# Kernel optimization log

Hardware: AMD Instinct MI355X
Metric: run time of the kernel (lower is better)

Reference implementation:

```python
import jax, jax.numpy as jnp
import numpy as np


def setup_inputs() -> dict:
    key = jax.random.key(0)
    k1, k2, k3, k4 = jax.random.split(key, 4)
    B1, N1, B2, N2, D = 64, 128, 64, 128, 128
    v1 = jax.random.normal(k1, (B1, N1, D), dtype=jnp.float32)
    v2 = jax.random.normal(k2, (B2, N2, D), dtype=jnp.float32)
    sz1 = jax.random.randint(k3, (B1,), 0, 128, dtype=jnp.int64)
    sz2 = jax.random.randint(k4, (B2,), 0, 128, dtype=jnp.int64)
    return {"v1": v1, "sz1": sz1, "v2": v2, "sz2": sz2}


def reference(v1, sz1, v2, sz2):
    # v1: (B1, N1, D) padded node features; v2: (B2, N2, D)
    # Pairwise Euclidean distances dist[b1,b2,i,j] = ||v1[b1,i] - v2[b2,j]||
    # via the gemm identity instead of the original's 5D broadcast.
    x2 = jnp.sum(v1 * v1, axis=-1)                     # (B1, N1)
    y2 = jnp.sum(v2 * v2, axis=-1)                     # (B2, N2)
    xy = jnp.einsum('aid,bjd->abij', v1, v2)           # (B1, B2, N1, N2)
    sq = x2[:, None, :, None] + y2[None, :, None, :] - 2.0 * xy
    dist = jnp.sqrt(jnp.maximum(sq, 0.0))              # (B1, B2, N1, N2)

    N1, N2 = v1.shape[1], v2.shape[1]
    mask1 = jnp.arange(N1)[None, :] >= sz1[:, None]    # (B1, N1) padded v1 nodes
    mask2 = jnp.arange(N2)[None, :] >= sz2[:, None]    # (B2, N2) padded v2 nodes
    mask = mask1[:, None, :, None] | mask2[None, :, None, :]  # (B1, B2, N1, N2)

    # Original fills masked entries with the global max of the (unmasked) distances.
    maximum = dist.max()
    dm = jnp.where(mask, maximum, dist)

    bm1 = dm.min(axis=2)                               # min over v1 nodes -> (B1, B2, N2)
    bm2 = dm.min(axis=3)                               # min over v2 nodes -> (B1, B2, N1)
    bm1 = jnp.where(jnp.all(mask, axis=2), 0.0, bm1)   # zero fully-masked columns
    bm2 = jnp.where(jnp.all(mask, axis=3), 0.0, bm2)   # zero fully-masked rows

    return bm1.sum(axis=2) + bm2.sum(axis=2)           # (B1, B2)
```

## Files before the change

### kernel.cpp

```cpp
#include <hip/hip_runtime.h>
#include <math.h>


typedef __attribute__((ext_vector_type(8))) short short8;
typedef __attribute__((ext_vector_type(4))) float f32x4;
typedef unsigned int u32;
typedef unsigned short ushort_t;

static __device__ __forceinline__ ushort_t f32_to_bf16_rne(float f) {
    u32 b = __float_as_uint(f);
    b += 0x7FFFu + ((b >> 16) & 1u);
    return (ushort_t)(b >> 16);
}

__global__ __launch_bounds__(256) void softhd_pre(
    const float* __restrict__ v1, const float* __restrict__ v2,
    ushort_t* __restrict__ v1b, ushort_t* __restrict__ v2b,
    float* __restrict__ x2g, float* __restrict__ y2g)
{
    int flat = blockIdx.x * 256 + threadIdx.x;
    int c = flat & 15;
    int r = (flat >> 4) & 127;
    int b = (flat >> 11) & 63;
    int t = flat >> 17;

    const float* src = (t ? v2 : v1) + ((size_t)((b << 7) + r) << 7) + c * 8;
    ushort_t* dst = (t ? v2b : v1b) + ((size_t)((b << 7) + r) << 7);

    float4 q0 = *(const float4*)(src);
    float4 q1 = *(const float4*)(src + 4);

    ushort_t h[8];
    h[0] = f32_to_bf16_rne(q0.x); h[1] = f32_to_bf16_rne(q0.y);
    h[2] = f32_to_bf16_rne(q0.z); h[3] = f32_to_bf16_rne(q0.w);
    h[4] = f32_to_bf16_rne(q1.x); h[5] = f32_to_bf16_rne(q1.y);
    h[6] = f32_to_bf16_rne(q1.z); h[7] = f32_to_bf16_rne(q1.w);

    float p = 0.f;
#pragma unroll
    for (int k = 0; k < 8; ++k) {
        float fv = __uint_as_float((u32)h[k] << 16);
        p += fv * fv;
    }

    uint4 w;
    w.x = (u32)h[0] | ((u32)h[1] << 16);
    w.y = (u32)h[2] | ((u32)h[3] << 16);
    w.z = (u32)h[4] | ((u32)h[5] << 16);
    w.w = (u32)h[6] | ((u32)h[7] << 16);
    *(uint4*)(dst + ((c ^ (r & 7)) << 3)) = w;

    p += __shfl_xor(p, 1);
    p += __shfl_xor(p, 2);
    p += __shfl_xor(p, 4);
    p += __shfl_xor(p, 8);
    if (c == 0) (t ? y2g : x2g)[(b << 7) + r] = p;
}

static __device__ __forceinline__ void stage_half(
    const char* g1, const char* g2, ushort_t* s1, ushort_t* s2,
    int tid, int srcoff)
{
#pragma unroll
    for (int it = 0; it < 4; ++it) {
        int m = it * 256 + tid;
        int so = ((m >> 3) << 8) + srcoff + ((m & 7) << 4);
        int dof = m << 4;
        __builtin_amdgcn_global_load_lds(
            (const __attribute__((address_space(1))) u32*)(g1 + so),
            (__attribute__((address_space(3))) u32*)((char*)s1 + dof),
            16, 0, 0);
        __builtin_amdgcn_global_load_lds(
            (const __attribute__((address_space(1))) u32*)(g2 + so),
            (__attribute__((address_space(3))) u32*)((char*)s2 + dof),
            16, 0, 0);
    }
}

__global__ __launch_bounds__(256, 3) void softhd_mfma(
    const ushort_t* __restrict__ v1b, const ushort_t* __restrict__ v2b,
    const float* __restrict__ x2g, const float* __restrict__ y2g,
    const int* __restrict__ sz1, const int* __restrict__ sz2,
    float* __restrict__ out)
{
    __shared__ __align__(16) ushort_t s1[128 * 64];
    __shared__ __align__(16) ushort_t s2[128 * 64];
    __shared__ float sx2[128], sy2[128];
    __shared__ u32 sbm1[128], sbm2[128];
    __shared__ float swsum[4];

    const int tid = threadIdx.x;
    const int lane = tid & 63;
    const int wid = tid >> 6;
    const int bid = ((blockIdx.x & 7) << 9) | (blockIdx.x >> 3);
    const int b1 = bid >> 6, b2 = bid & 63;

    const char* g1 = (const char*)(v1b + ((size_t)b1 << 14));
    const char* g2 = (const char*)(v2b + ((size_t)b2 << 14));

    stage_half(g1, g2, s1, s2, tid, 0);

    if (tid < 128) {
        sx2[tid] = x2g[(b1 << 7) + tid];
        sbm1[tid] = 0x7F800000u;
    } else {
        sy2[tid - 128] = y2g[(b2 << 7) + (tid - 128)];
        sbm2[tid - 128] = 0x7F800000u;
    }
    __syncthreads();

    const int qr = wid >> 1, qc = wid & 1;
    const int ibase = qr << 6, jbase = qc << 6;
    const int rf = lane & 15, kg = lane >> 4;
    const int h = rf & 7;

    const ushort_t* a_base = s1 + ((ibase + rf) << 6);
    const ushort_t* b_base = s2 + ((jbase + rf) << 6);

    f32x4 acc[4][4];
#pragma unroll
    for (int fi = 0; fi < 4; ++fi)
#pragma unroll
        for (int fj = 0; fj < 4; ++fj)
            acc[fi][fj] = (f32x4){0.f, 0.f, 0.f, 0.f};

#pragma unroll
    for (int half = 0; half < 2; ++half) {
        if (half == 1) {
            __syncthreads();
            stage_half(g1, g2, s1, s2, tid, 128);
            __syncthreads();
        }
#pragma unroll
        for (int s = 0; s < 2; ++s) {
            const int p8 = (((s << 2) + kg) ^ h) << 3;
            short8 a[4], b[4];
#pragma unroll
            for (int f = 0; f < 4; ++f) {
                a[f] = *(const short8*)(a_base + (f << 10) + p8);
                b[f] = *(const short8*)(b_base + (f << 10) + p8);
            }
#pragma unroll
            for (int fi = 0; fi < 4; ++fi)
#pragma unroll
                for (int fj = 0; fj < 4; ++fj)
                    acc[fi][fj] = __builtin_amdgcn_mfma_f32_16x16x32_bf16(
                        a[fi], b[fj], acc[fi][fj], 0, 0, 0);
        }
    }

    const int n1 = min(max(sz1[b1], 0), 128);
    const int n2 = min(max(sz2[b2], 0), 128);
    const float INF = __builtin_inff();

    float xie[16], yje[4];
#pragma unroll
    for (int t = 0; t < 16; ++t) {
        int i = ibase + ((t >> 2) << 4) + (kg << 2) + (t & 3);
        xie[t] = (i < n1) ? sx2[i] : INF;
    }
#pragma unroll
    for (int fj = 0; fj < 4; ++fj) {
        int j = jbase + (fj << 4) + rf;
        yje[fj] = (j < n2) ? sy2[j] : INF;
    }

    float minj[4], mini[16];
#pragma unroll
    for (int fj = 0; fj < 4; ++fj) minj[fj] = INF;
#pragma unroll
    for (int t = 0; t < 16; ++t) mini[t] = INF;

#pragma unroll
    for (int fi = 0; fi < 4; ++fi) {
        float u[4][4];
#pragma unroll
        for (int fj = 0; fj < 4; ++fj)
#pragma unroll
            for (int q = 0; q < 4; ++q)
                u[fj][q] = fmaf(acc[fi][fj][q], -2.f, xie[fi * 4 + q] + yje[fj]);
#pragma unroll
        for (int fj = 0; fj < 4; ++fj) {
            minj[fj] = fminf(fminf(minj[fj], u[fj][0]), u[fj][1]);
            minj[fj] = fminf(fminf(minj[fj], u[fj][2]), u[fj][3]);
        }
#pragma unroll
        for (int q = 0; q < 4; ++q) {
            float mt = mini[fi * 4 + q];
            mt = fminf(fminf(mt, u[0][q]), u[1][q]);
            mt = fminf(fminf(mt, u[2][q]), u[3][q]);
            mini[fi * 4 + q] = mt;
        }
    }

#pragma unroll
    for (int k = 0; k < 4; ++k) {
        const int d = 1 << k;
        const bool hi = (lane >> k) & 1;
#pragma unroll
        for (int base = 0; base < 16; base += 2 * (1 << k)) {
            float pa = fminf(mini[base], __shfl_xor(mini[base], d));
            float pb = fminf(mini[base + d], __shfl_xor(mini[base + d], d));
            mini[base] = hi ? pb : pa;
        }
    }
    {
        float dmin = __builtin_amdgcn_sqrtf(fmaxf(mini[0], 0.f));
        int i = ibase + ((rf >> 2) << 4) + (kg << 2) + (rf & 3);
        atomicMin(&sbm2[i], __float_as_uint(dmin));
    }

#pragma unroll
    for (int k = 0; k < 2; ++k) {
        const int d = 16 << k;
        const bool hi = (lane >> (4 + k)) & 1;
#pragma unroll
        for (int base = 0; base < 4; base += 2 * (1 << k)) {
            float pa = fminf(minj[base], __shfl_xor(minj[base], d));
            float pb = fminf(minj[base + (1 << k)],
                             __shfl_xor(minj[base + (1 << k)], d));
            minj[base] = hi ? pb : pa;
        }
    }
    {
        float dmin = __builtin_amdgcn_sqrtf(fmaxf(minj[0], 0.f));
        atomicMin(&sbm1[jbase + lane], __float_as_uint(dmin));
    }
    __syncthreads();

    float v = 0.f;
    if (tid < 128) {
        if (n1 > 0 && tid < n2) v += __uint_as_float(sbm1[tid]);
        if (n2 > 0 && tid < n1) v += __uint_as_float(sbm2[tid]);
    }
#pragma unroll
    for (int off = 32; off >= 1; off >>= 1) v += __shfl_down(v, off);
    if (lane == 0) swsum[wid] = v;
    __syncthreads();
    if (tid == 0) out[bid] = swsum[0] + swsum[1] + swsum[2] + swsum[3];
}

extern "C" void kernel_launch(void* const* d_in, const int* in_sizes, int n_in,
                              void* d_out, int out_size, void* d_ws, size_t ws_size,
                              hipStream_t stream) {
    const float* v1  = (const float*)d_in[0];
    const int*   sz1 = (const int*)d_in[1];
    const float* v2  = (const float*)d_in[2];
    const int*   sz2 = (const int*)d_in[3];
    float* out = (float*)d_out;
    (void)in_sizes; (void)n_in; (void)out_size; (void)ws_size;

    char* ws = (char*)d_ws;
    ushort_t* v1b = (ushort_t*)ws;
    ushort_t* v2b = (ushort_t*)(ws + (2u << 20));
    float*    x2g = (float*)(ws + (4u << 20));
    float*    y2g = x2g + 64 * 128;

    softhd_pre<<<dim3(1024), dim3(256), 0, stream>>>(v1, v2, v1b, v2b, x2g, y2g);
    softhd_mfma<<<dim3(4096), dim3(256), 0, stream>>>(v1b, v2b, x2g, y2g,
                                                      sz1, sz2, out);
}
```

Baseline: 36.55 us.

## Double-buffer K-quarter staging with chunk-major bf16 layout for overlapped LDS loads

The preprocessing kernel now writes bf16 features in a chunk-major layout, so each 32-wide K quarter of a 128-row tile is one contiguous 8KB block. The MFMA kernel splits K into four quarters held in a double-buffered LDS array. It issues the async global-to-LDS load for the next quarter before computing on the current one, which replaces the previous two-half, load-then-sync scheme. The occupancy hint is raised from 3 to 4 blocks, and the size loads are hoisted earlier. This trades more barriers per block for overlap of loads with MFMA work.

```diff
diff --git a/kernel.cpp b/kernel.cpp
--- a/kernel.cpp
+++ b/kernel.cpp
@@ -25,7 +25,7 @@
     int t = flat >> 17;
 
     const float* src = (t ? v2 : v1) + ((size_t)((b << 7) + r) << 7) + c * 8;
-    ushort_t* dst = (t ? v2b : v1b) + ((size_t)((b << 7) + r) << 7);
+    char* dstp = (char*)((t ? v2b : v1b) + ((size_t)b << 14));
 
     float4 q0 = *(const float4*)(src);
     float4 q1 = *(const float4*)(src + 4);
@@ -48,7 +48,9 @@
     w.y = (u32)h[2] | ((u32)h[3] << 16);
     w.z = (u32)h[4] | ((u32)h[5] << 16);
     w.w = (u32)h[6] | ((u32)h[7] << 16);
-    *(uint4*)(dst + ((c ^ (r & 7)) << 3)) = w;
+
+    int off = ((c >> 2) << 13) + ((r >> 3) << 9) + ((c & 3) << 7) + ((r & 7) << 4);
+    *(uint4*)(dstp + off) = w;
 
     p += __shfl_xor(p, 1);
     p += __shfl_xor(p, 2);
@@ -57,34 +59,13 @@
     if (c == 0) (t ? y2g : x2g)[(b << 7) + r] = p;
 }
 
-static __device__ __forceinline__ void stage_half(
-    const char* g1, const char* g2, ushort_t* s1, ushort_t* s2,
-    int tid, int srcoff)
-{
-#pragma unroll
-    for (int it = 0; it < 4; ++it) {
-        int m = it * 256 + tid;
-        int so = ((m >> 3) << 8) + srcoff + ((m & 7) << 4);
-        int dof = m << 4;
-        __builtin_amdgcn_global_load_lds(
-            (const __attribute__((address_space(1))) u32*)(g1 + so),
-            (__attribute__((address_space(3))) u32*)((char*)s1 + dof),
-            16, 0, 0);
-        __builtin_amdgcn_global_load_lds(
-            (const __attribute__((address_space(1))) u32*)(g2 + so),
-            (__attribute__((address_space(3))) u32*)((char*)s2 + dof),
-            16, 0, 0);
-    }
-}
-
-__global__ __launch_bounds__(256, 3) void softhd_mfma(
+__global__ __launch_bounds__(256, 4) void softhd_mfma(
     const ushort_t* __restrict__ v1b, const ushort_t* __restrict__ v2b,
     const float* __restrict__ x2g, const float* __restrict__ y2g,
     const int* __restrict__ sz1, const int* __restrict__ sz2,
     float* __restrict__ out)
 {
-    __shared__ __align__(16) ushort_t s1[128 * 64];
-    __shared__ __align__(16) ushort_t s2[128 * 64];
+    __shared__ __align__(16) ushort_t sb[2][2][4096];
     __shared__ float sx2[128], sy2[128];
     __shared__ u32 sbm1[128], sbm2[128];
     __shared__ float swsum[4];
@@ -95,10 +76,29 @@
     const int bid = ((blockIdx.x & 7) << 9) | (blockIdx.x >> 3);
     const int b1 = bid >> 6, b2 = bid & 63;
 
-    const char* g1 = (const char*)(v1b + ((size_t)b1 << 14));
-    const char* g2 = (const char*)(v2b + ((size_t)b2 << 14));
-
-    stage_half(g1, g2, s1, s2, tid, 0);
+    const char* gp0 = (const char*)(v1b + ((size_t)b1 << 14));
+    const char* gp1 = (const char*)(v2b + ((size_t)b2 << 14));
+
+#define STAGE(d, q)                                                          \
+    {                                                                        \
+        _Pragma("unroll")                                                    \
+        for (int e = 0; e < 2; ++e) {                                        \
+            int m16 = ((e << 8) + tid) << 4;                                 \
+            __builtin_amdgcn_global_load_lds(                                \
+                (const __attribute__((address_space(1))) u32*)(gp0 + ((q) << 13) + m16), \
+                (__attribute__((address_space(3))) u32*)((char*)&sb[d][0][0] + m16),     \
+                16, 0, 0);                                                   \
+            __builtin_amdgcn_global_load_lds(                                \
+                (const __attribute__((address_space(1))) u32*)(gp1 + ((q) << 13) + m16), \
+                (__attribute__((address_space(3))) u32*)((char*)&sb[d][1][0] + m16),     \
+                16, 0, 0);                                                   \
+        }                                                                    \
+    }
+
+    STAGE(0, 0);
+
+    const int n1 = min(max(sz1[b1], 0), 128);
+    const int n2 = min(max(sz2[b2], 0), 128);
 
     if (tid < 128) {
         sx2[tid] = x2g[(b1 << 7) + tid];
@@ -112,10 +112,15 @@
     const int qr = wid >> 1, qc = wid & 1;
     const int ibase = qr << 6, jbase = qc << 6;
     const int rf = lane & 15, kg = lane >> 4;
-    const int h = rf & 7;
-
-    const ushort_t* a_base = s1 + ((ibase + rf) << 6);
-    const ushort_t* b_base = s2 + ((jbase + rf) << 6);
+
+    int aoff[4], boff[4];
+#pragma unroll
+    for (int f = 0; f < 4; ++f) {
+        int ra = ibase + (f << 4) + rf;
+        int rb = jbase + (f << 4) + rf;
+        aoff[f] = ((ra >> 3) << 8) + (kg << 6) + ((ra & 7) << 3);
+        boff[f] = ((rb >> 3) << 8) + (kg << 6) + ((rb & 7) << 3);
+    }
 
     f32x4 acc[4][4];
 #pragma unroll
@@ -125,32 +130,25 @@
             acc[fi][fj] = (f32x4){0.f, 0.f, 0.f, 0.f};
 
 #pragma unroll
-    for (int half = 0; half < 2; ++half) {
-        if (half == 1) {
-            __syncthreads();
-            stage_half(g1, g2, s1, s2, tid, 128);
-            __syncthreads();
-        }
-#pragma unroll
-        for (int s = 0; s < 2; ++s) {
-            const int p8 = (((s << 2) + kg) ^ h) << 3;
-            short8 a[4], b[4];
-#pragma unroll
-            for (int f = 0; f < 4; ++f) {
-                a[f] = *(const short8*)(a_base + (f << 10) + p8);
-                b[f] = *(const short8*)(b_base + (f << 10) + p8);
-            }
-#pragma unroll
-            for (int fi = 0; fi < 4; ++fi)
-#pragma unroll
-                for (int fj = 0; fj < 4; ++fj)
-                    acc[fi][fj] = __builtin_amdgcn_mfma_f32_16x16x32_bf16(
-                        a[fi], b[fj], acc[fi][fj], 0, 0, 0);
-        }
-    }
-
-    const int n1 = min(max(sz1[b1], 0), 128);
-    const int n2 = min(max(sz2[b2], 0), 128);
+    for (int q = 0; q < 4; ++q) {
+        const int d = q & 1;
+        if (q < 3) STAGE(d ^ 1, q + 1);
+        short8 a[4], b[4];
+#pragma unroll
+        for (int f = 0; f < 4; ++f) {
+            a[f] = *(const short8*)(&sb[d][0][0] + aoff[f]);
+            b[f] = *(const short8*)(&sb[d][1][0] + boff[f]);
+        }
+#pragma unroll
+        for (int fi = 0; fi < 4; ++fi)
+#pragma unroll
+            for (int fj = 0; fj < 4; ++fj)
+                acc[fi][fj] = __builtin_amdgcn_mfma_f32_16x16x32_bf16(
+                    a[fi], b[fj], acc[fi][fj], 0, 0, 0);
+        __syncthreads();
+    }
+#undef STAGE
+
     const float INF = __builtin_inff();
 
     float xie[16], yje[4];
```

Result: no change. 36.55 us (+0.0%).
